# Kernel optimization log

Measured on AMD Instinct MI355X. Metric: run time of the kernel, lower is better.

The kernel has to match this reference:

```python
import jax, jax.numpy as jnp
import numpy as np

B, S, D = 4, 2048, 1024
E, K, H = 8, 2, 4096


def setup_inputs() -> dict:
    key = jax.random.key(0)
    ks = jax.random.split(key, 8)
    sd = 1.0 / np.sqrt(D)
    sh = 1.0 / np.sqrt(H)
    x = jax.random.normal(ks[0], (B, S, D), dtype=jnp.float32)
    gate_w = jax.random.normal(ks[1], (D, E), dtype=jnp.float32) * sd
    gate_b = jnp.zeros((E,), dtype=jnp.float32)
    w1 = jax.random.normal(ks[2], (E, D, H), dtype=jnp.float32) * sd
    b1 = jnp.zeros((E, H), dtype=jnp.float32)
    w2 = jax.random.normal(ks[3], (E, H, D), dtype=jnp.float32) * sh
    b2 = jnp.zeros((E, D), dtype=jnp.float32)
    return {"x": x, "gate_w": gate_w, "gate_b": gate_b,
            "w1": w1, "b1": b1, "w2": w2, "b2": b2}


def reference(x, gate_w, gate_b, w1, b1, w2, b2):
    # gate logits [B,S,E]
    logits = jnp.einsum('bsd,de->bse', x, gate_w) + gate_b
    # top-k over experts, softmax over the k selected (dim=2), in float32
    weights, selected = jax.lax.top_k(logits, K)            # [B,S,K]
    weights = jax.nn.softmax(weights.astype(jnp.float32), axis=-1).astype(x.dtype)
    out = jnp.zeros_like(x)
    for i in range(E):
        # per-token combine weight for expert i (0 if not routed here)
        w_i = jnp.sum(jnp.where(selected == i, weights, 0.0), axis=-1)  # [B,S]
        h = jax.nn.gelu(jnp.einsum('bsd,dh->bsh', x, w1[i]) + b1[i])    # [B,S,H]
        y = jnp.einsum('bsh,hd->bsd', h, w2[i]) + b2[i]                  # [B,S,D]
        out = out + w_i[..., None] * y
    return out
```

## Files before the change

### kernel.cpp

```cpp
#include <hip/hip_runtime.h>
#include <hip/hip_bf16.h>
#include <stdint.h>

#define T_TOK 8192
#define D_DIM 1024
#define E_NUM 8
#define H_DIM 4096
#define NPAD 144
#define PPX (NPAD / 8)
#define GATEB 2048
#define TRB1 2048
#define TRB2 2048

typedef short bf16x8 __attribute__((ext_vector_type(8)));
typedef float f32x4 __attribute__((ext_vector_type(4)));
typedef unsigned short usv8 __attribute__((ext_vector_type(8)));

#define AS1 __attribute__((address_space(1)))
#define AS3 __attribute__((address_space(3)))

__device__ __forceinline__ unsigned short f2b(float f) {
  union { float f; uint32_t u; } v; v.f = f;
  uint32_t r = (v.u + 0x7fffu + ((v.u >> 16) & 1u)) >> 16;
  return (unsigned short)r;
}

__device__ __forceinline__ float gelu_tanh(float x) {
  float u = 0.7978845608028654f * (x + 0.044715f * x * x * x);
  u = fminf(fmaxf(u, -15.f), 15.f);
  float e = __expf(2.f * u);
  float t = (e - 1.f) / (e + 1.f);
  return 0.5f * x * (1.f + t);
}

__device__ __forceinline__ void gload_lds16(const void* g, void* l) {
  __builtin_amdgcn_global_load_lds((const AS1 uint32_t*)g, (AS3 uint32_t*)l, 16, 0, 0);
}

__device__ __forceinline__ void transpose_tile(const float* __restrict__ in,
                                               unsigned short* __restrict__ outp,
                                               int R, int C, int r0, int c0,
                                               unsigned short (*tile)[260], int t) {
  int sc = (t & 15) * 4;
  int srb = (t >> 4) * 4;
#pragma unroll
  for (int it = 0; it < 4; ++it) {
    int sr = srb + it * 64;
    float4 v0 = *(const float4*)(in + (size_t)(r0 + sr + 0) * C + c0 + sc);
    float4 v1 = *(const float4*)(in + (size_t)(r0 + sr + 1) * C + c0 + sc);
    float4 v2 = *(const float4*)(in + (size_t)(r0 + sr + 2) * C + c0 + sc);
    float4 v3 = *(const float4*)(in + (size_t)(r0 + sr + 3) * C + c0 + sc);
    ushort4 o;
    o.x = f2b(v0.x); o.y = f2b(v1.x); o.z = f2b(v2.x); o.w = f2b(v3.x);
    *(ushort4*)&tile[sc + 0][sr] = o;
    o.x = f2b(v0.y); o.y = f2b(v1.y); o.z = f2b(v2.y); o.w = f2b(v3.y);
    *(ushort4*)&tile[sc + 1][sr] = o;
    o.x = f2b(v0.z); o.y = f2b(v1.z); o.z = f2b(v2.z); o.w = f2b(v3.z);
    *(ushort4*)&tile[sc + 2][sr] = o;
    o.x = f2b(v0.w); o.y = f2b(v1.w); o.z = f2b(v2.w); o.w = f2b(v3.w);
    *(ushort4*)&tile[sc + 3][sr] = o;
  }
  __syncthreads();
  int wv = t >> 6, lane = t & 63;
  int rowHalf = lane >> 5, el = (lane & 31) * 8;
#pragma unroll
  for (int it = 0; it < 8; ++it) {
    int orow = wv * 16 + it * 2 + rowHalf;
    usv8 o = *(const usv8*)&tile[orow][el];
    *(usv8*)(outp + (size_t)(c0 + orow) * R + r0 + el) = o;
  }
}

__global__ __launch_bounds__(256) void moe_prep(const float* __restrict__ x,
                                                const float* __restrict__ gw,
                                                const float* __restrict__ gb,
                                                const float* __restrict__ w1,
                                                const float* __restrict__ b2,
                                                unsigned short* __restrict__ xb,
                                                unsigned short* __restrict__ w1t,
                                                int2* __restrict__ sel,
                                                float2* __restrict__ wts,
                                                int* __restrict__ meta,
                                                float* __restrict__ out) {
  __shared__ unsigned short tile[64][260];
  int z = blockIdx.x;
  if (z >= GATEB) {
    int z2 = z - GATEB;
    int e = z2 >> 8, bx = z2 & 255;
    transpose_tile(w1 + (size_t)e * D_DIM * H_DIM, w1t + (size_t)e * D_DIM * H_DIM,
                   D_DIM, H_DIM, (bx >> 6) * 256, (bx & 63) * 64, tile, threadIdx.x);
    return;
  }
  int lane = threadIdx.x & 63;
  int t = z * 4 + (threadIdx.x >> 6);
  const float* xr = x + (size_t)t * D_DIM;
  unsigned short* xo = xb + (size_t)t * D_DIM;
  float acc[8];
#pragma unroll
  for (int e = 0; e < 8; e++) acc[e] = 0.f;
#pragma unroll
  for (int i = 0; i < 4; i++) {
    int d0 = lane * 4 + i * 256;
    float4 xv = *(const float4*)(xr + d0);
    ushort4 o;
    o.x = f2b(xv.x); o.y = f2b(xv.y); o.z = f2b(xv.z); o.w = f2b(xv.w);
    *(ushort4*)(xo + d0) = o;
    const float* gp = gw + (size_t)d0 * 8;
    float xs[4] = {xv.x, xv.y, xv.z, xv.w};
#pragma unroll
    for (int j = 0; j < 4; j++) {
#pragma unroll
      for (int e = 0; e < 8; e++) acc[e] += xs[j] * gp[j * 8 + e];
    }
  }
#pragma unroll
  for (int off = 32; off > 0; off >>= 1) {
#pragma unroll
    for (int e = 0; e < 8; e++) acc[e] += __shfl_xor(acc[e], off);
  }
  float lg[8];
#pragma unroll
  for (int e = 0; e < 8; e++) lg[e] = acc[e] + gb[e];
  int e0 = 0; float b0v = lg[0];
#pragma unroll
  for (int e = 1; e < 8; e++) if (lg[e] > b0v) { b0v = lg[e]; e0 = e; }
  int e1 = -1; float b1v = -1e30f;
#pragma unroll
  for (int e = 0; e < 8; e++) if (e != e0 && lg[e] > b1v) { b1v = lg[e]; e1 = e; }
  float d = __expf(b1v - b0v);
  float w0 = 1.f / (1.f + d), w1v = d / (1.f + d);
  if (lane == 0) {
    sel[t] = make_int2(e0, e1);
    wts[t] = make_float2(w0, w1v);
    atomicAdd(&meta[e0], 1);
    atomicAdd(&meta[e1], 1);
  }
  const float* ba = b2 + (size_t)e0 * D_DIM;
  const float* bb = b2 + (size_t)e1 * D_DIM;
  float* orow = out + (size_t)t * D_DIM;
#pragma unroll
  for (int k = 0; k < 4; k++) {
    int dd = lane * 4 + k * 256;
    float4 a = *(const float4*)(ba + dd);
    float4 b = *(const float4*)(bb + dd);
    float4 o;
    o.x = w0 * a.x + w1v * b.x;
    o.y = w0 * a.y + w1v * b.y;
    o.z = w0 * a.z + w1v * b.z;
    o.w = w0 * a.w + w1v * b.w;
    *(float4*)(orow + dd) = o;
  }
}

__global__ __launch_bounds__(256) void moe_scatter(const int2* __restrict__ sel,
                                                   const float2* __restrict__ wts,
                                                   int* __restrict__ meta,
                                                   int* __restrict__ token_id,
                                                   float* __restrict__ weightv) {
  int t = blockIdx.x * 256 + threadIdx.x;
  if (t >= T_TOK) return;
  int cnt[8];
#pragma unroll
  for (int e = 0; e < 8; e++) cnt[e] = meta[e];
  int2 s = sel[t];
  float2 w = wts[t];
  int o0 = 0, o1 = 0;
#pragma unroll
  for (int e = 0; e < 8; e++) {
    if (e < s.x) o0 += cnt[e];
    if (e < s.y) o1 += cnt[e];
  }
  int p0 = o0 + atomicAdd(&meta[20 + s.x], 1); token_id[p0] = t; weightv[p0] = w.x;
  int p1 = o1 + atomicAdd(&meta[20 + s.y], 1); token_id[p1] = t; weightv[p1] = w.y;
}

__device__ __forceinline__ bool panel_decode(const int* __restrict__ meta, int wi,
                                             int& e, int& m0, int& seg, int& ne) {
  int acc = 0, pre = 0;
  e = -1;
#pragma unroll
  for (int k = 0; k < 8; k++) {
    int ck = meta[k];
    int nb = (ck + 127) >> 7;
    if (wi >= acc && wi < acc + nb) { e = k; m0 = (wi - acc) << 7; seg = pre; ne = ck; }
    acc += nb; pre += ck;
  }
  return e >= 0;
}

__global__ __launch_bounds__(256, 4) void moe_gemm1(const unsigned short* __restrict__ xb,
                                                    const unsigned short* __restrict__ w1t,
                                                    const float* __restrict__ b1,
                                                    const float* __restrict__ w2,
                                                    unsigned short* __restrict__ w2t,
                                                    const int* __restrict__ meta,
                                                    const int* __restrict__ token_id,
                                                    unsigned short* __restrict__ hbuf) {
  __shared__ unsigned short SH[16640];
  int z = blockIdx.x;
  if (z < TRB2) {
    int e = z >> 8, bx = z & 255;
    transpose_tile(w2 + (size_t)e * H_DIM * D_DIM, w2t + (size_t)e * H_DIM * D_DIM,
                   H_DIM, D_DIM, (bx >> 4) * 256, (bx & 15) * 64,
                   (unsigned short (*)[260])SH, threadIdx.x);
    return;
  }
  int b = z - TRB2;
  int c = b & 7, u = b >> 3;
  int n = u & 31, ps = u >> 5;
  int e, m0, seg, ne;
  if (!panel_decode(meta, c * PPX + ps, e, m0, seg, ne)) return;
  int n0 = n * 128;
  const unsigned short* wB = w1t + (size_t)e * H_DIM * D_DIM;

  unsigned short (*As)[4096] = (unsigned short (*)[4096])SH;
  unsigned short (*Bs)[4096] = (unsigned short (*)[4096])(SH + 8192);

  int tid = threadIdx.x, lane = tid & 63, wv = tid >> 6;
  const unsigned short* aptr[2];
  const unsigned short* bptr[2];
#pragma unroll
  for (int q = 0; q < 2; q++) {
    int chunk = tid + q * 256;
    int row = chunk >> 2;
    int ko = ((chunk & 3) ^ ((chunk >> 3) & 3)) * 8;
    int gi = m0 + row; if (gi >= ne) gi = m0;
    int tok = token_id[seg + gi];
    aptr[q] = xb + (size_t)tok * D_DIM + ko;
    bptr[q] = wB + (size_t)(n0 + row) * D_DIM + ko;
  }
  auto stage = [&](int buf, int kt) {
#pragma unroll
    for (int q = 0; q < 2; q++) {
      gload_lds16(aptr[q] + kt * 32, &As[buf][(wv + 4 * q) * 512]);
      gload_lds16(bptr[q] + kt * 32, &Bs[buf][(wv + 4 * q) * 512]);
    }
  };

  f32x4 acc[4][4] = {};
  int wr = wv >> 1, wc = wv & 1;
  int sswz = ((lane >> 4) ^ ((lane >> 1) & 3)) * 8;
  int abase = (wr * 64 + (lane & 15)) * 32 + sswz;
  int bbase = (wc * 64 + (lane & 15)) * 32 + sswz;

  stage(0, 0);
  __syncthreads();
  const int nk = D_DIM / 32;
  for (int kt = 0; kt < nk; ++kt) {
    int cur = kt & 1;
    if (kt + 1 < nk) stage(cur ^ 1, kt + 1);
    bf16x8 af[4], bfr[4];
#pragma unroll
    for (int m = 0; m < 4; m++) af[m] = *(const bf16x8*)&As[cur][abase + m * 512];
#pragma unroll
    for (int nn = 0; nn < 4; nn++) bfr[nn] = *(const bf16x8*)&Bs[cur][bbase + nn * 512];
#pragma unroll
    for (int m = 0; m < 4; m++)
#pragma unroll
      for (int nn = 0; nn < 4; nn++)
        acc[m][nn] = __builtin_amdgcn_mfma_f32_16x16x32_bf16(af[m], bfr[nn], acc[m][nn], 0, 0, 0);
    __syncthreads();
  }

  int rbase = wr * 64 + (lane >> 4) * 4;
  int cbase = n0 + wc * 64 + (lane & 15);
  const float* b1e = b1 + (size_t)e * H_DIM + cbase;
  float bv[4];
#pragma unroll
  for (int nn = 0; nn < 4; nn++) bv[nn] = b1e[nn * 16];
#pragma unroll
  for (int m = 0; m < 4; m++) {
#pragma unroll
    for (int j = 0; j < 4; j++) {
      int gi = m0 + rbase + m * 16 + j;
      if (gi < ne) {
        unsigned short* hrow = hbuf + (size_t)(seg + gi) * H_DIM + cbase;
#pragma unroll
        for (int nn = 0; nn < 4; nn++) {
          float v = acc[m][nn][j] + bv[nn];
          hrow[nn * 16] = f2b(gelu_tanh(v));
        }
      }
    }
  }
}

__global__ __launch_bounds__(256, 4) void moe_gemm2(const unsigned short* __restrict__ hbuf,
                                                    const unsigned short* __restrict__ w2t,
                                                    const int* __restrict__ meta,
                                                    const int* __restrict__ token_id,
                                                    const float* __restrict__ weightv,
                                                    float* __restrict__ out) {
  int b = blockIdx.x;
  int c = b & 7, u = b >> 3;
  int n = u & 7, ks = (u >> 3) & 1, ps = u >> 4;
  int e, m0, seg, ne;
  if (!panel_decode(meta, c * PPX + ps, e, m0, seg, ne)) return;
  int n0 = n * 128;
  int kbase = ks * 2048;
  const unsigned short* wB = w2t + (size_t)e * D_DIM * H_DIM;

  __shared__ unsigned short As[2][4096];
  __shared__ unsigned short Bs[2][4096];

  int tid = threadIdx.x, lane = tid & 63, wv = tid >> 6;
  const unsigned short* aptr[2];
  const unsigned short* bptr[2];
#pragma unroll
  for (int q = 0; q < 2; q++) {
    int chunk = tid + q * 256;
    int row = chunk >> 2;
    int ko = ((chunk & 3) ^ ((chunk >> 3) & 3)) * 8;
    int gi = m0 + row; if (gi >= ne) gi = m0;
    aptr[q] = hbuf + (size_t)(seg + gi) * H_DIM + kbase + ko;
    bptr[q] = wB + (size_t)(n0 + row) * H_DIM + kbase + ko;
  }
  auto stage = [&](int buf, int kt) {
#pragma unroll
    for (int q = 0; q < 2; q++) {
      gload_lds16(aptr[q] + kt * 32, &As[buf][(wv + 4 * q) * 512]);
      gload_lds16(bptr[q] + kt * 32, &Bs[buf][(wv + 4 * q) * 512]);
    }
  };

  f32x4 acc[4][4] = {};
  int wr = wv >> 1, wc = wv & 1;
  int sswz = ((lane >> 4) ^ ((lane >> 1) & 3)) * 8;
  int abase = (wr * 64 + (lane & 15)) * 32 + sswz;
  int bbase = (wc * 64 + (lane & 15)) * 32 + sswz;

  stage(0, 0);
  __syncthreads();
  const int nk = 2048 / 32;
  for (int kt = 0; kt < nk; ++kt) {
    int cur = kt & 1;
    if (kt + 1 < nk) stage(cur ^ 1, kt + 1);
    bf16x8 af[4], bfr[4];
#pragma unroll
    for (int m = 0; m < 4; m++) af[m] = *(const bf16x8*)&As[cur][abase + m * 512];
#pragma unroll
    for (int nn = 0; nn < 4; nn++) bfr[nn] = *(const bf16x8*)&Bs[cur][bbase + nn * 512];
#pragma unroll
    for (int m = 0; m < 4; m++)
#pragma unroll
      for (int nn = 0; nn < 4; nn++)
        acc[m][nn] = __builtin_amdgcn_mfma_f32_16x16x32_bf16(af[m], bfr[nn], acc[m][nn], 0, 0, 0);
    __syncthreads();
  }

  int rbase = wr * 64 + (lane >> 4) * 4;
  int cbase = n0 + wc * 64 + (lane & 15);
#pragma unroll
  for (int m = 0; m < 4; m++) {
#pragma unroll
    for (int j = 0; j < 4; j++) {
      int gi = m0 + rbase + m * 16 + j;
      if (gi < ne) {
        int p = seg + gi;
        int tok = token_id[p];
        float wt = weightv[p];
        float* orow = out + (size_t)tok * D_DIM + cbase;
#pragma unroll
        for (int nn = 0; nn < 4; nn++)
          atomicAdd(&orow[nn * 16], wt * acc[m][nn][j]);
      }
    }
  }
}

extern "C" void kernel_launch(void* const* d_in, const int* in_sizes, int n_in,
                              void* d_out, int out_size, void* d_ws, size_t ws_size,
                              hipStream_t stream) {
  const float* x      = (const float*)d_in[0];
  const float* gate_w = (const float*)d_in[1];
  const float* gate_b = (const float*)d_in[2];
  const float* w1     = (const float*)d_in[3];
  const float* b1     = (const float*)d_in[4];
  const float* w2     = (const float*)d_in[5];
  const float* b2     = (const float*)d_in[6];
  float* out = (float*)d_out;

  uint8_t* ws = (uint8_t*)d_ws;
  unsigned short* hbuf = (unsigned short*)(ws);
  unsigned short* xb   = (unsigned short*)(ws + 134217728ull);
  unsigned short* w1t  = (unsigned short*)(ws + 150994944ull);
  unsigned short* w2t  = (unsigned short*)(ws + 218103808ull);
  int*    token_id = (int*)  (ws + 285212672ull);
  float*  weightv  = (float*)(ws + 285278208ull);
  float2* wts      = (float2*)(ws + 285343744ull);
  int2*   sel      = (int2*) (ws + 285409280ull);
  int*    meta     = (int*)  (ws + 285474816ull);

  hipMemsetAsync(meta, 0, 128, stream);

  moe_prep<<<dim3(GATEB + TRB1), 256, 0, stream>>>(
      x, gate_w, gate_b, w1, b2, xb, w1t, sel, wts, meta, out);
  moe_scatter<<<dim3(T_TOK / 256), 256, 0, stream>>>(sel, wts, meta, token_id, weightv);

  moe_gemm1<<<dim3(TRB2 + NPAD * 32), 256, 0, stream>>>(
      xb, w1t, b1, w2, w2t, meta, token_id, hbuf);
  moe_gemm2<<<dim3(NPAD * 16), 256, 0, stream>>>(hbuf, w2t, meta, token_id, weightv, out);
}
```

Baseline: 793.3 us.

## Split gating from w1 transpose and fuse scatter with transpose and bias init

The memset is replaced by a tiny init kernel that zeroes the counters and transposes the gate weights so each expert's column can be read with vectorized float4 loads. The gate kernel now only does bf16 conversion, gate logits and top-2 selection, with the selection done by lane 0 alone. The w1 transpose, the token scatter and the b2-weighted output initialisation move into one combined launch. This rebalances work across launches and removes a memset, but adds one extra tiny launch and runs the w1 transpose after gating instead of alongside it.

```diff
diff --git a/kernel.cpp b/kernel.cpp
--- a/kernel.cpp
+++ b/kernel.cpp
@@ -71,28 +71,27 @@
   }
 }
 
-__global__ __launch_bounds__(256) void moe_prep(const float* __restrict__ x,
-                                                const float* __restrict__ gw,
+__global__ void moe_init(const float* __restrict__ gw, float* __restrict__ gwT,
+                         int* __restrict__ meta) {
+  int t = threadIdx.x;
+  if (t < 32) meta[t] = 0;
+#pragma unroll
+  for (int k = 0; k < 32; ++k) {
+    int g = t * 32 + k;
+    int d = g >> 3, e = g & 7;
+    gwT[e * 1024 + d] = gw[g];
+  }
+}
+
+__global__ __launch_bounds__(256) void moe_gate(const float* __restrict__ x,
+                                                const float* __restrict__ gwT,
                                                 const float* __restrict__ gb,
-                                                const float* __restrict__ w1,
-                                                const float* __restrict__ b2,
                                                 unsigned short* __restrict__ xb,
-                                                unsigned short* __restrict__ w1t,
                                                 int2* __restrict__ sel,
                                                 float2* __restrict__ wts,
-                                                int* __restrict__ meta,
-                                                float* __restrict__ out) {
-  __shared__ unsigned short tile[64][260];
-  int z = blockIdx.x;
-  if (z >= GATEB) {
-    int z2 = z - GATEB;
-    int e = z2 >> 8, bx = z2 & 255;
-    transpose_tile(w1 + (size_t)e * D_DIM * H_DIM, w1t + (size_t)e * D_DIM * H_DIM,
-                   D_DIM, H_DIM, (bx >> 6) * 256, (bx & 63) * 64, tile, threadIdx.x);
-    return;
-  }
+                                                int* __restrict__ meta) {
   int lane = threadIdx.x & 63;
-  int t = z * 4 + (threadIdx.x >> 6);
+  int t = blockIdx.x * 4 + (threadIdx.x >> 6);
   const float* xr = x + (size_t)t * D_DIM;
   unsigned short* xo = xb + (size_t)t * D_DIM;
   float acc[8];
@@ -105,12 +104,10 @@
     ushort4 o;
     o.x = f2b(xv.x); o.y = f2b(xv.y); o.z = f2b(xv.z); o.w = f2b(xv.w);
     *(ushort4*)(xo + d0) = o;
-    const float* gp = gw + (size_t)d0 * 8;
-    float xs[4] = {xv.x, xv.y, xv.z, xv.w};
-#pragma unroll
-    for (int j = 0; j < 4; j++) {
-#pragma unroll
-      for (int e = 0; e < 8; e++) acc[e] += xs[j] * gp[j * 8 + e];
+#pragma unroll
+    for (int e = 0; e < 8; e++) {
+      float4 gv = *(const float4*)(gwT + e * 1024 + d0);
+      acc[e] += xv.x * gv.x + xv.y * gv.y + xv.z * gv.z + xv.w * gv.w;
     }
   }
 #pragma unroll
@@ -118,60 +115,72 @@
 #pragma unroll
     for (int e = 0; e < 8; e++) acc[e] += __shfl_xor(acc[e], off);
   }
-  float lg[8];
-#pragma unroll
-  for (int e = 0; e < 8; e++) lg[e] = acc[e] + gb[e];
-  int e0 = 0; float b0v = lg[0];
-#pragma unroll
-  for (int e = 1; e < 8; e++) if (lg[e] > b0v) { b0v = lg[e]; e0 = e; }
-  int e1 = -1; float b1v = -1e30f;
-#pragma unroll
-  for (int e = 0; e < 8; e++) if (e != e0 && lg[e] > b1v) { b1v = lg[e]; e1 = e; }
-  float d = __expf(b1v - b0v);
-  float w0 = 1.f / (1.f + d), w1v = d / (1.f + d);
   if (lane == 0) {
+    float lg[8];
+#pragma unroll
+    for (int e = 0; e < 8; e++) lg[e] = acc[e] + gb[e];
+    int e0 = 0; float b0v = lg[0];
+#pragma unroll
+    for (int e = 1; e < 8; e++) if (lg[e] > b0v) { b0v = lg[e]; e0 = e; }
+    int e1 = -1; float b1v = -1e30f;
+#pragma unroll
+    for (int e = 0; e < 8; e++) if (e != e0 && lg[e] > b1v) { b1v = lg[e]; e1 = e; }
+    float d = __expf(b1v - b0v);
+    float w0 = 1.f / (1.f + d), w1v = d / (1.f + d);
     sel[t] = make_int2(e0, e1);
     wts[t] = make_float2(w0, w1v);
     atomicAdd(&meta[e0], 1);
     atomicAdd(&meta[e1], 1);
   }
-  const float* ba = b2 + (size_t)e0 * D_DIM;
-  const float* bb = b2 + (size_t)e1 * D_DIM;
-  float* orow = out + (size_t)t * D_DIM;
-#pragma unroll
-  for (int k = 0; k < 4; k++) {
-    int dd = lane * 4 + k * 256;
-    float4 a = *(const float4*)(ba + dd);
-    float4 b = *(const float4*)(bb + dd);
-    float4 o;
-    o.x = w0 * a.x + w1v * b.x;
-    o.y = w0 * a.y + w1v * b.y;
-    o.z = w0 * a.z + w1v * b.z;
-    o.w = w0 * a.w + w1v * b.w;
-    *(float4*)(orow + dd) = o;
-  }
-}
-
-__global__ __launch_bounds__(256) void moe_scatter(const int2* __restrict__ sel,
-                                                   const float2* __restrict__ wts,
-                                                   int* __restrict__ meta,
-                                                   int* __restrict__ token_id,
-                                                   float* __restrict__ weightv) {
-  int t = blockIdx.x * 256 + threadIdx.x;
-  if (t >= T_TOK) return;
-  int cnt[8];
-#pragma unroll
-  for (int e = 0; e < 8; e++) cnt[e] = meta[e];
+}
+
+__global__ __launch_bounds__(256) void moe_scatter2(const float* __restrict__ w1,
+                                                    unsigned short* __restrict__ w1t,
+                                                    const int2* __restrict__ sel,
+                                                    const float2* __restrict__ wts,
+                                                    const float* __restrict__ b2,
+                                                    int* __restrict__ meta,
+                                                    int* __restrict__ token_id,
+                                                    float* __restrict__ weightv,
+                                                    float* __restrict__ out) {
+  __shared__ __align__(16) unsigned short tile[64][260];
+  int z = blockIdx.x;
+  if (z < TRB1) {
+    int e = z >> 8, bx = z & 255;
+    transpose_tile(w1 + (size_t)e * D_DIM * H_DIM, w1t + (size_t)e * D_DIM * H_DIM,
+                   D_DIM, H_DIM, (bx >> 6) * 256, (bx & 63) * 64, tile, threadIdx.x);
+    return;
+  }
+  if (z < TRB1 + 32) {
+    int t = (z - TRB1) * 256 + threadIdx.x;
+    if (t >= T_TOK) return;
+    int cnt[8];
+#pragma unroll
+    for (int e = 0; e < 8; e++) cnt[e] = meta[e];
+    int2 s = sel[t];
+    float2 w = wts[t];
+    int o0 = 0, o1 = 0;
+#pragma unroll
+    for (int e = 0; e < 8; e++) {
+      if (e < s.x) o0 += cnt[e];
+      if (e < s.y) o1 += cnt[e];
+    }
+    int p0 = o0 + atomicAdd(&meta[20 + s.x], 1); token_id[p0] = t; weightv[p0] = w.x;
+    int p1 = o1 + atomicAdd(&meta[20 + s.y], 1); token_id[p1] = t; weightv[p1] = w.y;
+    return;
+  }
+  int t = z - (TRB1 + 32);
+  int d = threadIdx.x * 4;
   int2 s = sel[t];
   float2 w = wts[t];
-  int o0 = 0, o1 = 0;
-#pragma unroll
-  for (int e = 0; e < 8; e++) {
-    if (e < s.x) o0 += cnt[e];
-    if (e < s.y) o1 += cnt[e];
-  }
-  int p0 = o0 + atomicAdd(&meta[20 + s.x], 1); token_id[p0] = t; weightv[p0] = w.x;
-  int p1 = o1 + atomicAdd(&meta[20 + s.y], 1); token_id[p1] = t; weightv[p1] = w.y;
+  float4 a = *(const float4*)(b2 + (size_t)s.x * D_DIM + d);
+  float4 b = *(const float4*)(b2 + (size_t)s.y * D_DIM + d);
+  float4 o;
+  o.x = w.x * a.x + w.y * b.x;
+  o.y = w.x * a.y + w.y * b.y;
+  o.z = w.x * a.z + w.y * b.z;
+  o.w = w.x * a.w + w.y * b.w;
+  *(float4*)(out + (size_t)t * D_DIM + d) = o;
 }
 
 __device__ __forceinline__ bool panel_decode(const int* __restrict__ meta, int wi,
@@ -196,7 +205,7 @@
                                                     const int* __restrict__ meta,
                                                     const int* __restrict__ token_id,
                                                     unsigned short* __restrict__ hbuf) {
-  __shared__ unsigned short SH[16640];
+  __shared__ __align__(16) unsigned short SH[16640];
   int z = blockIdx.x;
   if (z < TRB2) {
     int e = z >> 8, bx = z & 255;
@@ -390,13 +399,12 @@
   float2* wts      = (float2*)(ws + 285343744ull);
   int2*   sel      = (int2*) (ws + 285409280ull);
   int*    meta     = (int*)  (ws + 285474816ull);
-
-  hipMemsetAsync(meta, 0, 128, stream);
-
-  moe_prep<<<dim3(GATEB + TRB1), 256, 0, stream>>>(
-      x, gate_w, gate_b, w1, b2, xb, w1t, sel, wts, meta, out);
-  moe_scatter<<<dim3(T_TOK / 256), 256, 0, stream>>>(sel, wts, meta, token_id, weightv);
-
+  float*  gwT      = (float*)(ws + 285475328ull);
+
+  moe_init<<<dim3(1), 256, 0, stream>>>(gate_w, gwT, meta);
+  moe_gate<<<dim3(GATEB), 256, 0, stream>>>(x, gwT, gate_b, xb, sel, wts, meta);
+  moe_scatter2<<<dim3(TRB1 + 32 + T_TOK), 256, 0, stream>>>(
+      w1, w1t, sel, wts, b2, meta, token_id, weightv, out);
   moe_gemm1<<<dim3(TRB2 + NPAD * 32), 256, 0, stream>>>(
       xb, w1t, b1, w2, w2t, meta, token_id, hbuf);
   moe_gemm2<<<dim3(NPAD * 16), 256, 0, stream>>>(hbuf, w2t, meta, token_id, weightv, out);
```

Result: no change. 790.4 us (-0.4%).
